# Kernel optimization log

Hardware: AMD Instinct MI355X
Metric: run time of the kernel (lower is better)

## Reference

```python
import jax, jax.numpy as jnp
import numpy as np

K = 512
H = 8

def setup_inputs() -> dict:
    key = jax.random.key(0)
    k1, k2, k3, k4, k5 = jax.random.split(key, 5)
    b, s = 2, 2048
    x = jax.random.normal(k1, (b, s, K), dtype=jnp.float32)
    # torch Linear weights: shape [out_features, in_features]
    scale = 0.02
    Wq = jax.random.normal(k2, (H * K, K), dtype=jnp.float32) * scale
    Wk = jax.random.normal(k3, (H * K, K), dtype=jnp.float32) * scale
    Wv = jax.random.normal(k4, (H * K, K), dtype=jnp.float32) * scale
    Wu = jax.random.normal(k5, (K, H * K), dtype=jnp.float32) * scale
    return {"x": x, "Wq": Wq, "Wk": Wk, "Wv": Wv, "Wu": Wu}

def reference(x, Wq, Wk, Wv, Wu):
    b, s, _ = x.shape
    # project and split heads: [b, h, s, k]
    q = jnp.einsum('bsd,hed->bhse', x, Wq.reshape(H, K, K))
    kk = jnp.einsum('bsd,hed->bhse', x, Wk.reshape(H, K, K))
    v = jnp.einsum('bsd,hed->bhse', x, Wv.reshape(H, K, K))
    scale = K ** (-0.25)
    dot = jnp.einsum('bhse,bhte->bhst', q * scale, kk * scale)  # [b,h,s,s]
    causal = jnp.tril(jnp.ones((s, s), dtype=bool))
    dot = jnp.where(causal[None, None], dot, -jnp.inf)
    weights = jax.nn.softmax(dot, axis=-1)
    heads_out = jnp.einsum('bhst,bhte->bhse', weights, v)  # [b,h,s,k]
    heads_out = heads_out.transpose(0, 2, 1, 3).reshape(b, s, H * K)
    return heads_out @ Wu.T
```

## Files before the change

### kernel.cpp

```cpp
#include <hip/hip_runtime.h>
#include <hip/hip_bf16.h>
#include <cstdint>
#include <cstddef>


typedef __bf16 bf16;
typedef __bf16 bf16x8 __attribute__((ext_vector_type(8)));
typedef float  f32x4  __attribute__((ext_vector_type(4)));
typedef unsigned short u16x4 __attribute__((ext_vector_type(4)));

__device__ __forceinline__ void gl2lds16(const void* g, void* l) {
  __builtin_amdgcn_global_load_lds(
      (const __attribute__((address_space(1))) unsigned int*)g,
      (__attribute__((address_space(3))) unsigned int*)l, 16, 0, 0);
}

__device__ __forceinline__ unsigned short bfbits(float f) {
  return __builtin_bit_cast(unsigned short, (__bf16)f);
}

__global__ __launch_bounds__(256) void cvt_all(
    const float* __restrict__ x,  const float* __restrict__ wq,
    const float* __restrict__ wk, const float* __restrict__ wv,
    const float* __restrict__ wu,
    bf16* __restrict__ xb,  bf16* __restrict__ wqb, bf16* __restrict__ wkb,
    bf16* __restrict__ wvb, bf16* __restrict__ wub)
{
  const int Q4 = (1 << 21) / 4;
  int i = blockIdx.x * 256 + threadIdx.x;
  int a = i / Q4;
  int off = (i - a * Q4) * 4;
  const float* s; bf16* d;
  switch (a) {
    case 0: s = x;  d = xb;  break;
    case 1: s = wq; d = wqb; break;
    case 2: s = wk; d = wkb; break;
    case 3: s = wv; d = wvb; break;
    default: s = wu; d = wub; break;
  }
  float4 v = *(const float4*)(s + off);
  u16x4 o = { bfbits(v.x), bfbits(v.y), bfbits(v.z), bfbits(v.w) };
  *(u16x4*)(d + off) = o;
}

template<int BM, int BN, int MODE>
__global__ __launch_bounds__((BM >= 256 ? 2 : BM / 64) * (BN / 64) * 64)
void gemm_bt(const bf16* __restrict__ A, const bf16* __restrict__ B,
             void* __restrict__ Cp, int M, int N, int K)
{
  constexpr int BK = 32;
  constexpr int WM = (BM >= 256 ? 128 : 64);
  constexpr int MI = WM / 16;
  constexpr int WAVES_M = BM / WM;
  constexpr int WAVES_N = BN / 64;
  constexpr int NT = WAVES_M * WAVES_N * 64;
  __shared__ __align__(16) bf16 lds[2][(BM + BN) * BK];

  const int tid = threadIdx.x, w = tid >> 6, lane = tid & 63;
  const int g = lane >> 4, c16 = lane & 15;
  const int q8 = gridDim.x >> 3;
  const int wg = (blockIdx.x & 7) * q8 + (blockIdx.x >> 3);
  const int nbn = N / BN;
  const int bm = wg / nbn, bn = wg % nbn;
  const int m0 = bm * BM, n0 = bn * BN;
  const int wr = w / WAVES_N, wc = w % WAVES_N;

  f32x4 z = {0.f, 0.f, 0.f, 0.f};
  f32x4 acc[MI][4];
  #pragma unroll
  for (int i = 0; i < MI; i++)
    #pragma unroll
    for (int j = 0; j < 4; j++) acc[i][j] = z;

  const int nk = K / BK;

  auto stage = [&](int buf, int kt) {
    bf16* la = &lds[buf][0];
    #pragma unroll
    for (int r = 0; r < (BM * BK / 8) / NT; r++) {
      int c = r * NT + tid;
      int row = c >> 2, p = c & 3, s = p ^ ((row >> 1) & 3);
      gl2lds16(A + (size_t)(m0 + row) * K + (size_t)kt * BK + s * 8,
               la + (r * NT + w * 64) * 8);
    }
    bf16* lb = &lds[buf][BM * BK];
    #pragma unroll
    for (int r = 0; r < (BN * BK / 8) / NT; r++) {
      int c = r * NT + tid;
      int row = c >> 2, p = c & 3, s = p ^ ((row >> 1) & 3);
      gl2lds16(B + (size_t)(n0 + row) * K + (size_t)kt * BK + s * 8,
               lb + (r * NT + w * 64) * 8);
    }
  };

  stage(0, 0);
  __syncthreads();
  int cur = 0;
  for (int kt = 0; kt < nk; ++kt) {
    if (kt + 1 < nk) stage(cur ^ 1, kt + 1);
    const bf16* lA = &lds[cur][0];
    const bf16* lB = &lds[cur][BM * BK];
    bf16x8 af[MI], bfv[4];
    #pragma unroll
    for (int i = 0; i < MI; i++) {
      int ra = wr * WM + i * 16 + c16;
      af[i] = *(const bf16x8*)&lA[ra * BK + ((g ^ ((ra >> 1) & 3)) * 8)];
    }
    #pragma unroll
    for (int j = 0; j < 4; j++) {
      int rb = wc * 64 + j * 16 + c16;
      bfv[j] = *(const bf16x8*)&lB[rb * BK + ((g ^ ((rb >> 1) & 3)) * 8)];
    }
    #pragma unroll
    for (int i = 0; i < MI; i++)
      #pragma unroll
      for (int j = 0; j < 4; j++)
        acc[i][j] = __builtin_amdgcn_mfma_f32_16x16x32_bf16(af[i], bfv[j],
                                                            acc[i][j], 0, 0, 0);
    __syncthreads();
    cur ^= 1;
  }

  if constexpr (MODE == 0) {
    bf16* C = (bf16*)Cp;
    #pragma unroll
    for (int i = 0; i < MI; i++) {
      int mg = m0 + wr * WM + i * 16 + g * 4;
      #pragma unroll
      for (int j = 0; j < 4; j++) {
        int ng = n0 + wc * 64 + j * 16 + c16;
        #pragma unroll
        for (int jj = 0; jj < 4; jj++)
          C[(size_t)(mg + jj) * N + ng] = (bf16)acc[i][j][jj];
      }
    }
  } else if constexpr (MODE == 1) {
    bf16* C = (bf16*)Cp;
    #pragma unroll
    for (int i = 0; i < MI; i++) {
      int mg = m0 + wr * WM + i * 16 + g * 4;
      int bb = mg >> 11, srow = mg & 2047;
      #pragma unroll
      for (int j = 0; j < 4; j++) {
        int ng = n0 + wc * 64 + j * 16 + c16;
        u16x4 pk = { bfbits(acc[i][j][0]), bfbits(acc[i][j][1]),
                     bfbits(acc[i][j][2]), bfbits(acc[i][j][3]) };
        *(u16x4*)&C[(size_t)(bb * 4096 + ng) * 2048 + srow] = pk;
      }
    }
  } else {
    float* C = (float*)Cp;
    #pragma unroll
    for (int i = 0; i < MI; i++) {
      int mg = m0 + wr * WM + i * 16 + g * 4;
      #pragma unroll
      for (int j = 0; j < 4; j++) {
        int ng = n0 + wc * 64 + j * 16 + c16;
        #pragma unroll
        for (int jj = 0; jj < 4; jj++)
          C[(size_t)(mg + jj) * N + ng] = acc[i][j][jj];
      }
    }
  }
}

__global__ __launch_bounds__(512)
void sgemm_causal(const bf16* __restrict__ Qb, const bf16* __restrict__ Kb,
                  bf16* __restrict__ Sp, float* __restrict__ l)
{
  constexpr int BK = 32;
  __shared__ __align__(16) bf16 lds[2][512 * BK];
  const int tid = threadIdx.x, w = tid >> 6, lane = tid & 63;
  const int g = lane >> 4, c16 = lane & 15;

  const int wg = (blockIdx.x & 7) * 72 + (blockIdx.x >> 3);
  const int bh = wg / 36, t = wg % 36;
  int TM = 0;
  while ((TM + 1) * (TM + 2) / 2 <= t) TM++;
  const int TN = t - TM * (TM + 1) / 2;
  const int b = bh >> 3, h = bh & 7;
  const bf16* Ab = Qb + (size_t)(b * 2048 + TM * 256) * 4096 + h * 512;
  const bf16* Bb = Kb + (size_t)(b * 2048 + TN * 256) * 4096 + h * 512;
  const int wr = w >> 2, wc = w & 3;

  f32x4 z = {0.f, 0.f, 0.f, 0.f};
  f32x4 acc[8][4];
  #pragma unroll
  for (int i = 0; i < 8; i++)
    #pragma unroll
    for (int j = 0; j < 4; j++) acc[i][j] = z;

  auto stage = [&](int buf, int kt) {
    bf16* la = &lds[buf][0];
    #pragma unroll
    for (int r = 0; r < 2; r++) {
      int c = r * 512 + tid;
      int row = c >> 2, p = c & 3, s = p ^ ((row >> 1) & 3);
      gl2lds16(Ab + (size_t)row * 4096 + kt * BK + s * 8,
               la + (r * 512 + w * 64) * 8);
    }
    bf16* lb = &lds[buf][256 * BK];
    #pragma unroll
    for (int r = 0; r < 2; r++) {
      int c = r * 512 + tid;
      int row = c >> 2, p = c & 3, s = p ^ ((row >> 1) & 3);
      gl2lds16(Bb + (size_t)row * 4096 + kt * BK + s * 8,
               lb + (r * 512 + w * 64) * 8);
    }
  };

  stage(0, 0);
  __syncthreads();
  int cur = 0;
  for (int kt = 0; kt < 16; ++kt) {
    if (kt + 1 < 16) stage(cur ^ 1, kt + 1);
    const bf16* lA = &lds[cur][0];
    const bf16* lB = &lds[cur][256 * BK];
    bf16x8 af[8], bfv[4];
    #pragma unroll
    for (int i = 0; i < 8; i++) {
      int ra = wr * 128 + i * 16 + c16;
      af[i] = *(const bf16x8*)&lA[ra * BK + ((g ^ ((ra >> 1) & 3)) * 8)];
    }
    #pragma unroll
    for (int j = 0; j < 4; j++) {
      int rb = wc * 64 + j * 16 + c16;
      bfv[j] = *(const bf16x8*)&lB[rb * BK + ((g ^ ((rb >> 1) & 3)) * 8)];
    }
    #pragma unroll
    for (int i = 0; i < 8; i++)
      #pragma unroll
      for (int j = 0; j < 4; j++)
        acc[i][j] = __builtin_amdgcn_mfma_f32_16x16x32_bf16(af[i], bfv[j],
                                                            acc[i][j], 0, 0, 0);
    __syncthreads();
    cur ^= 1;
  }

  const float SC2 = 0.044194173824159216f * 1.4426950408889634f;
  bf16* spb = Sp + (size_t)bh * 136 * 16384;
  float rsum[8][4];
  #pragma unroll
  for (int i = 0; i < 8; i++)
    #pragma unroll
    for (int jj = 0; jj < 4; jj++) rsum[i][jj] = 0.f;

  #pragma unroll
  for (int i = 0; i < 8; i++) {
    #pragma unroll
    for (int j = 0; j < 4; j++) {
      int kl = wc * 64 + j * 16 + c16;
      int kglob = TN * 256 + kl;
      int tn128 = kglob >> 7, kc = kglob & 127;
      #pragma unroll
      for (int jj = 0; jj < 4; jj++) {
        int ml = wr * 128 + i * 16 + g * 4 + jj;
        int qglob = TM * 256 + ml;
        float p = (kglob <= qglob) ? exp2f(acc[i][j][jj] * SC2) : 0.f;
        rsum[i][jj] += p;
        int tm128 = qglob >> 7;
        if (tn128 <= tm128)
          spb[(size_t)(tm128 * (tm128 + 1) / 2 + tn128) * 16384
              + (qglob & 127) * 128 + kc] = (bf16)p;
      }
    }
  }
  #pragma unroll
  for (int i = 0; i < 8; i++)
    #pragma unroll
    for (int jj = 0; jj < 4; jj++) {
      float v = rsum[i][jj];
      v += __shfl_xor(v, 1);
      v += __shfl_xor(v, 2);
      v += __shfl_xor(v, 4);
      v += __shfl_xor(v, 8);
      if (c16 == 0) {
        int qglob = TM * 256 + wr * 128 + i * 16 + g * 4 + jj;
        atomicAdd(&l[bh * 2048 + qglob], v);
      }
    }
}

__global__ __launch_bounds__(512)
void pv_gemm(const bf16* __restrict__ Pp, const bf16* __restrict__ Vt,
             const float* __restrict__ l, bf16* __restrict__ HO)
{
  constexpr int BK = 32;
  __shared__ __align__(16) bf16 lds[2][384 * BK];
  __shared__ float sInv[128];
  const int tid = threadIdx.x, w = tid >> 6, lane = tid & 63;
  const int g = lane >> 4, c16 = lane & 15;

  const int wg = (blockIdx.x & 7) * 64 + (blockIdx.x >> 3);
  const int bh = wg >> 5, r5 = wg & 31;
  const int tm = 15 - (r5 >> 1), nd = r5 & 1;
  const int b = bh >> 3, h = bh & 7;
  const size_t pb = (size_t)bh * 136 + (size_t)tm * (tm + 1) / 2;
  const bf16* Bb = Vt + (size_t)(bh * 512 + nd * 256) * 2048;
  const int wr = w >> 2, wc = w & 3;
  const int nk = (tm + 1) * 4;

  f32x4 z = {0.f, 0.f, 0.f, 0.f};
  f32x4 acc[4][4];
  #pragma unroll
  for (int i = 0; i < 4; i++)
    #pragma unroll
    for (int j = 0; j < 4; j++) acc[i][j] = z;

  auto stage = [&](int buf, int kt) {
    const bf16* At = Pp + (pb + (kt >> 2)) * 16384 + (kt & 3) * 32;
    bf16* la = &lds[buf][0];
    {
      int row = tid >> 2, p = tid & 3, s = p ^ ((row >> 1) & 3);
      gl2lds16(At + (size_t)row * 128 + s * 8, la + (w * 64) * 8);
    }
    bf16* lb = &lds[buf][128 * BK];
    #pragma unroll
    for (int r = 0; r < 2; r++) {
      int c = r * 512 + tid;
      int row = c >> 2, p = c & 3, s = p ^ ((row >> 1) & 3);
      gl2lds16(Bb + (size_t)row * 2048 + kt * BK + s * 8,
               lb + (r * 512 + w * 64) * 8);
    }
  };

  stage(0, 0);
  if (tid < 128) sInv[tid] = 1.0f / l[bh * 2048 + tm * 128 + tid];
  __syncthreads();
  int cur = 0;
  for (int kt = 0; kt < nk; ++kt) {
    if (kt + 1 < nk) stage(cur ^ 1, kt + 1);
    const bf16* lA = &lds[cur][0];
    const bf16* lB = &lds[cur][128 * BK];
    bf16x8 af[4], bfv[4];
    #pragma unroll
    for (int i = 0; i < 4; i++) {
      int ra = wr * 64 + i * 16 + c16;
      af[i] = *(const bf16x8*)&lA[ra * BK + ((g ^ ((ra >> 1) & 3)) * 8)];
    }
    #pragma unroll
    for (int j = 0; j < 4; j++) {
      int rb = wc * 64 + j * 16 + c16;
      bfv[j] = *(const bf16x8*)&lB[rb * BK + ((g ^ ((rb >> 1) & 3)) * 8)];
    }
    #pragma unroll
    for (int i = 0; i < 4; i++)
      #pragma unroll
      for (int j = 0; j < 4; j++)
        acc[i][j] = __builtin_amdgcn_mfma_f32_16x16x32_bf16(af[i], bfv[j],
                                                            acc[i][j], 0, 0, 0);
    __syncthreads();
    cur ^= 1;
  }

  bf16* Cb = HO + (size_t)(b * 2048 + tm * 128) * 4096 + h * 512 + nd * 256;
  #pragma unroll
  for (int i = 0; i < 4; i++) {
    int ml = wr * 64 + i * 16 + g * 4;
    #pragma unroll
    for (int j = 0; j < 4; j++) {
      int nl = wc * 64 + j * 16 + c16;
      #pragma unroll
      for (int jj = 0; jj < 4; jj++)
        Cb[(size_t)(ml + jj) * 4096 + nl] =
            (bf16)(acc[i][j][jj] * sInv[ml + jj]);
    }
  }
}

extern "C" void kernel_launch(void* const* d_in, const int* in_sizes, int n_in,
                              void* d_out, int out_size, void* d_ws,
                              size_t ws_size, hipStream_t stream)
{
  (void)in_sizes; (void)n_in; (void)out_size; (void)ws_size;
  const float* x  = (const float*)d_in[0];
  const float* wq = (const float*)d_in[1];
  const float* wk = (const float*)d_in[2];
  const float* wv = (const float*)d_in[3];
  const float* wu = (const float*)d_in[4];

  char* ws = (char*)d_ws;
  const size_t MB = 1024 * 1024;
  bf16*  wub = (bf16*)(ws + 0 * MB);
  float* lR  = (float*)(ws + 4 * MB);
  bf16*  Qb  = (bf16*)(ws + 5 * MB);
  bf16*  Kbf = (bf16*)(ws + 37 * MB);
  bf16*  Sp  = (bf16*)(ws + 69 * MB);
  bf16*  wqb = (bf16*)(ws + 69 * MB);
  bf16*  wkb = (bf16*)(ws + 73 * MB);
  bf16*  xb  = (bf16*)(ws + 137 * MB);
  bf16*  wvb = (bf16*)(ws + 141 * MB);
  bf16*  Vtb = Kbf;
  bf16*  HOb = Qb;

  hipMemsetAsync(lR, 0, 16 * 2048 * sizeof(float), stream);
  hipLaunchKernelGGL(cvt_all, dim3(10240), dim3(256), 0, stream,
                     x, wq, wk, wv, wu, xb, wqb, wkb, wvb, wub);
  hipLaunchKernelGGL((gemm_bt<256, 256, 0>), dim3(256), dim3(512), 0, stream,
                     xb, wqb, (void*)Qb, 4096, 4096, 512);
  hipLaunchKernelGGL((gemm_bt<256, 256, 0>), dim3(256), dim3(512), 0, stream,
                     xb, wkb, (void*)Kbf, 4096, 4096, 512);
  hipLaunchKernelGGL(sgemm_causal, dim3(576), dim3(512), 0, stream,
                     Qb, Kbf, Sp, lR);
  hipLaunchKernelGGL((gemm_bt<256, 256, 1>), dim3(256), dim3(512), 0, stream,
                     xb, wvb, (void*)Vtb, 4096, 4096, 512);
  hipLaunchKernelGGL(pv_gemm, dim3(512), dim3(512), 0, stream,
                     Sp, Vtb, lR, HOb);
  hipLaunchKernelGGL((gemm_bt<128, 64, 2>), dim3(256), dim3(128), 0, stream,
                     HOb, wub, d_out, 4096, 512, 4096);
}
```

Before: 371.7 us.

## Stage GEMM epilogues through LDS for coalesced vector global stores

The projection GEMM, QK^T/softmax and PV kernels now write accumulator tiles into padded shared memory, in half-tiles, and then copy them out with 16-byte row-contiguous global stores. Before, each lane wrote scattered 2- or 4-byte elements, which made poorly coalesced store traffic for the large Q/K/V, P and head-output buffers. The shared buffer is sized to the larger of the staging and epilogue needs, and the extra barriers add synchronisation cost. The final output projection GEMM also changes its tile shape from 128x64 to 64x128, which now covers 128 columns per block.

```diff
diff --git a/kernel.cpp b/kernel.cpp
--- a/kernel.cpp
+++ b/kernel.cpp
@@ -54,7 +54,12 @@
   constexpr int WAVES_M = BM / WM;
   constexpr int WAVES_N = BN / 64;
   constexpr int NT = WAVES_M * WAVES_N * 64;
-  __shared__ __align__(16) bf16 lds[2][(BM + BN) * BK];
+  constexpr int STG = 2 * (BM + BN) * BK;
+  constexpr int EPE = (MODE == 0) ? 128 * 264
+                    : (MODE == 1) ? 256 * 136
+                    : 64 * 132 * 2;
+  constexpr int SME = STG > EPE ? STG : EPE;
+  __shared__ __align__(16) bf16 smem[SME];
 
   const int tid = threadIdx.x, w = tid >> 6, lane = tid & 63;
   const int g = lane >> 4, c16 = lane & 15;
@@ -75,7 +80,7 @@
   const int nk = K / BK;
 
   auto stage = [&](int buf, int kt) {
-    bf16* la = &lds[buf][0];
+    bf16* la = &smem[buf * (BM + BN) * BK];
     #pragma unroll
     for (int r = 0; r < (BM * BK / 8) / NT; r++) {
       int c = r * NT + tid;
@@ -83,7 +88,7 @@
       gl2lds16(A + (size_t)(m0 + row) * K + (size_t)kt * BK + s * 8,
                la + (r * NT + w * 64) * 8);
     }
-    bf16* lb = &lds[buf][BM * BK];
+    bf16* lb = &smem[buf * (BM + BN) * BK + BM * BK];
     #pragma unroll
     for (int r = 0; r < (BN * BK / 8) / NT; r++) {
       int c = r * NT + tid;
@@ -98,8 +103,8 @@
   int cur = 0;
   for (int kt = 0; kt < nk; ++kt) {
     if (kt + 1 < nk) stage(cur ^ 1, kt + 1);
-    const bf16* lA = &lds[cur][0];
-    const bf16* lB = &lds[cur][BM * BK];
+    const bf16* lA = &smem[cur * (BM + BN) * BK];
+    const bf16* lB = &smem[cur * (BM + BN) * BK + BM * BK];
     bf16x8 af[MI], bfv[4];
     #pragma unroll
     for (int i = 0; i < MI; i++) {
@@ -122,44 +127,87 @@
   }
 
   if constexpr (MODE == 0) {
+    bf16* ep = smem;
+    #pragma unroll
+    for (int hp = 0; hp < 2; ++hp) {
+      if (wr == hp) {
+        #pragma unroll
+        for (int i = 0; i < MI; i++) {
+          int rl = i * 16 + g * 4;
+          #pragma unroll
+          for (int j = 0; j < 4; j++) {
+            int cl = wc * 64 + j * 16 + c16;
+            #pragma unroll
+            for (int jj = 0; jj < 4; jj++)
+              ep[(rl + jj) * 264 + cl] = (bf16)acc[i][j][jj];
+          }
+        }
+      }
+      __syncthreads();
+      {
+        bf16* C = (bf16*)Cp;
+        int r = tid >> 2, ch = tid & 3;
+        const bf16* src = &ep[r * 264 + ch * 64];
+        bf16* dst = C + (size_t)(m0 + hp * 128 + r) * N + n0 + ch * 64;
+        #pragma unroll
+        for (int q = 0; q < 8; q++)
+          *(bf16x8*)(dst + q * 8) = *(const bf16x8*)(src + q * 8);
+      }
+      if (hp == 0) __syncthreads();
+    }
+  } else if constexpr (MODE == 1) {
+    bf16* ep = smem;
     bf16* C = (bf16*)Cp;
     #pragma unroll
+    for (int hp = 0; hp < 2; ++hp) {
+      if (wr == hp) {
+        #pragma unroll
+        for (int i = 0; i < MI; i++) {
+          int rl = i * 16 + g * 4;
+          #pragma unroll
+          for (int j = 0; j < 4; j++) {
+            int cl = wc * 64 + j * 16 + c16;
+            u16x4 pk = { bfbits(acc[i][j][0]), bfbits(acc[i][j][1]),
+                         bfbits(acc[i][j][2]), bfbits(acc[i][j][3]) };
+            *(u16x4*)&ep[cl * 136 + rl] = pk;
+          }
+        }
+      }
+      __syncthreads();
+      {
+        int cl = tid >> 1, rc = tid & 1;
+        const bf16* src = &ep[cl * 136 + rc * 64];
+        int mg = m0 + hp * 128 + rc * 64;
+        int bb = mg >> 11, srow = mg & 2047;
+        bf16* dst = C + ((size_t)(bb * 4096 + n0 + cl)) * 2048 + srow;
+        #pragma unroll
+        for (int q = 0; q < 8; q++)
+          *(bf16x8*)(dst + q * 8) = *(const bf16x8*)(src + q * 8);
+      }
+      if (hp == 0) __syncthreads();
+    }
+  } else {
+    float* ep = (float*)smem;
+    #pragma unroll
     for (int i = 0; i < MI; i++) {
-      int mg = m0 + wr * WM + i * 16 + g * 4;
+      int rl = i * 16 + g * 4;
       #pragma unroll
       for (int j = 0; j < 4; j++) {
-        int ng = n0 + wc * 64 + j * 16 + c16;
+        int cl = wc * 64 + j * 16 + c16;
         #pragma unroll
         for (int jj = 0; jj < 4; jj++)
-          C[(size_t)(mg + jj) * N + ng] = (bf16)acc[i][j][jj];
-      }
-    }
-  } else if constexpr (MODE == 1) {
-    bf16* C = (bf16*)Cp;
-    #pragma unroll
-    for (int i = 0; i < MI; i++) {
-      int mg = m0 + wr * WM + i * 16 + g * 4;
-      int bb = mg >> 11, srow = mg & 2047;
-      #pragma unroll
-      for (int j = 0; j < 4; j++) {
-        int ng = n0 + wc * 64 + j * 16 + c16;
-        u16x4 pk = { bfbits(acc[i][j][0]), bfbits(acc[i][j][1]),
-                     bfbits(acc[i][j][2]), bfbits(acc[i][j][3]) };
-        *(u16x4*)&C[(size_t)(bb * 4096 + ng) * 2048 + srow] = pk;
-      }
-    }
-  } else {
-    float* C = (float*)Cp;
-    #pragma unroll
-    for (int i = 0; i < MI; i++) {
-      int mg = m0 + wr * WM + i * 16 + g * 4;
-      #pragma unroll
-      for (int j = 0; j < 4; j++) {
-        int ng = n0 + wc * 64 + j * 16 + c16;
-        #pragma unroll
-        for (int jj = 0; jj < 4; jj++)
-          C[(size_t)(mg + jj) * N + ng] = acc[i][j][jj];
-      }
+          ep[(rl + jj) * 132 + cl] = acc[i][j][jj];
+      }
+    }
+    __syncthreads();
+    {
+      float* C = (float*)Cp;
+      int r = tid >> 1, ch = tid & 1;
+      const float* src = &ep[r * 132 + ch * 64];
+      float* dst = C + (size_t)(m0 + r) * N + n0 + ch * 64;
+      #pragma unroll
+      for (int q = 0; q < 16; q++)
+        *(float4*)(dst + q * 4) = *(const float4*)(src + q * 4);
     }
   }
 }
@@ -169,7 +217,9 @@
                   bf16* __restrict__ Sp, float* __restrict__ l)
 {
   constexpr int BK = 32;
-  __shared__ __align__(16) bf16 lds[2][512 * BK];
+  constexpr int STG = 2 * 512 * BK;
+  constexpr int EPE = 128 * 264;
+  __shared__ __align__(16) bf16 smem[EPE > STG ? EPE : STG];
   const int tid = threadIdx.x, w = tid >> 6, lane = tid & 63;
   const int g = lane >> 4, c16 = lane & 15;
 
@@ -191,7 +241,7 @@
     for (int j = 0; j < 4; j++) acc[i][j] = z;
 
   auto stage = [&](int buf, int kt) {
-    bf16* la = &lds[buf][0];
+    bf16* la = &smem[buf * 16384];
     #pragma unroll
     for (int r = 0; r < 2; r++) {
       int c = r * 512 + tid;
@@ -199,7 +249,7 @@
       gl2lds16(Ab + (size_t)row * 4096 + kt * BK + s * 8,
                la + (r * 512 + w * 64) * 8);
     }
-    bf16* lb = &lds[buf][256 * BK];
+    bf16* lb = &smem[buf * 16384 + 256 * BK];
     #pragma unroll
     for (int r = 0; r < 2; r++) {
       int c = r * 512 + tid;
@@ -214,8 +264,8 @@
   int cur = 0;
   for (int kt = 0; kt < 16; ++kt) {
     if (kt + 1 < 16) stage(cur ^ 1, kt + 1);
-    const bf16* lA = &lds[cur][0];
-    const bf16* lB = &lds[cur][256 * BK];
+    const bf16* lA = &smem[cur * 16384];
+    const bf16* lB = &smem[cur * 16384 + 256 * BK];
     bf16x8 af[8], bfv[4];
     #pragma unroll
     for (int i = 0; i < 8; i++) {
@@ -239,6 +289,7 @@
 
   const float SC2 = 0.044194173824159216f * 1.4426950408889634f;
   bf16* spb = Sp + (size_t)bh * 136 * 16384;
+  bf16* ep = smem;
   float rsum[8][4];
   #pragma unroll
   for (int i = 0; i < 8; i++)
@@ -246,25 +297,41 @@
     for (int jj = 0; jj < 4; jj++) rsum[i][jj] = 0.f;
 
   #pragma unroll
-  for (int i = 0; i < 8; i++) {
-    #pragma unroll
-    for (int j = 0; j < 4; j++) {
-      int kl = wc * 64 + j * 16 + c16;
-      int kglob = TN * 256 + kl;
-      int tn128 = kglob >> 7, kc = kglob & 127;
-      #pragma unroll
-      for (int jj = 0; jj < 4; jj++) {
-        int ml = wr * 128 + i * 16 + g * 4 + jj;
-        int qglob = TM * 256 + ml;
-        float p = (kglob <= qglob) ? exp2f(acc[i][j][jj] * SC2) : 0.f;
-        rsum[i][jj] += p;
-        int tm128 = qglob >> 7;
-        if (tn128 <= tm128)
-          spb[(size_t)(tm128 * (tm128 + 1) / 2 + tn128) * 16384
-              + (qglob & 127) * 128 + kc] = (bf16)p;
-      }
-    }
-  }
+  for (int hp = 0; hp < 2; ++hp) {
+    if (wr == hp) {
+      #pragma unroll
+      for (int i = 0; i < 8; i++) {
+        #pragma unroll
+        for (int j = 0; j < 4; j++) {
+          int cl = wc * 64 + j * 16 + c16;
+          int kglob = TN * 256 + cl;
+          #pragma unroll
+          for (int jj = 0; jj < 4; jj++) {
+            int rl = i * 16 + g * 4 + jj;
+            int qglob = TM * 256 + hp * 128 + rl;
+            float p = (kglob <= qglob) ? exp2f(acc[i][j][jj] * SC2) : 0.f;
+            rsum[i][jj] += p;
+            ep[rl * 264 + cl] = (bf16)p;
+          }
+        }
+      }
+    }
+    __syncthreads();
+    {
+      int r = tid >> 2, ch = tid & 3;
+      int tm128 = 2 * TM + hp, tn128 = 2 * TN + (ch >> 1);
+      if (tn128 <= tm128) {
+        const bf16* src = &ep[r * 264 + ch * 64];
+        bf16* dst = spb + (size_t)(tm128 * (tm128 + 1) / 2 + tn128) * 16384
+                    + r * 128 + (ch & 1) * 64;
+        #pragma unroll
+        for (int q = 0; q < 8; q++)
+          *(bf16x8*)(dst + q * 8) = *(const bf16x8*)(src + q * 8);
+      }
+    }
+    if (hp == 0) __syncthreads();
+  }
+
   #pragma unroll
   for (int i = 0; i < 8; i++)
     #pragma unroll
@@ -286,7 +353,8 @@
              const float* __restrict__ l, bf16* __restrict__ HO)
 {
   constexpr int BK = 32;
-  __shared__ __align__(16) bf16 lds[2][384 * BK];
+  constexpr int STG = 2 * 384 * BK;
+  __shared__ __align__(16) bf16 smem[STG];
   __shared__ float sInv[128];
   const int tid = threadIdx.x, w = tid >> 6, lane = tid & 63;
   const int g = lane >> 4, c16 = lane & 15;
@@ -294,7 +362,7 @@
   const int wg = (blockIdx.x & 7) * 64 + (blockIdx.x >> 3);
   const int bh = wg >> 5, r5 = wg & 31;
   const int tm = 15 - (r5 >> 1), nd = r5 & 1;
-  const int b = bh >> 3, h = bh & 7;
+  const int b = bh >> 3, hh = bh & 7;
   const size_t pb = (size_t)bh * 136 + (size_t)tm * (tm + 1) / 2;
   const bf16* Bb = Vt + (size_t)(bh * 512 + nd * 256) * 2048;
   const int wr = w >> 2, wc = w & 3;
@@ -309,12 +377,12 @@
 
   auto stage = [&](int buf, int kt) {
     const bf16* At = Pp + (pb + (kt >> 2)) * 16384 + (kt & 3) * 32;
-    bf16* la = &lds[buf][0];
+    bf16* la = &smem[buf * 12288];
     {
       int row = tid >> 2, p = tid & 3, s = p ^ ((row >> 1) & 3);
       gl2lds16(At + (size_t)row * 128 + s * 8, la + (w * 64) * 8);
     }
-    bf16* lb = &lds[buf][128 * BK];
+    bf16* lb = &smem[buf * 12288 + 128 * BK];
     #pragma unroll
     for (int r = 0; r < 2; r++) {
       int c = r * 512 + tid;
@@ -330,8 +398,8 @@
   int cur = 0;
   for (int kt = 0; kt < nk; ++kt) {
     if (kt + 1 < nk) stage(cur ^ 1, kt + 1);
-    const bf16* lA = &lds[cur][0];
-    const bf16* lB = &lds[cur][128 * BK];
+    const bf16* lA = &smem[cur * 12288];
+    const bf16* lB = &smem[cur * 12288 + 128 * BK];
     bf16x8 af[4], bfv[4];
     #pragma unroll
     for (int i = 0; i < 4; i++) {
@@ -353,18 +421,35 @@
     cur ^= 1;
   }
 
-  bf16* Cb = HO + (size_t)(b * 2048 + tm * 128) * 4096 + h * 512 + nd * 256;
-  #pragma unroll
-  for (int i = 0; i < 4; i++) {
-    int ml = wr * 64 + i * 16 + g * 4;
-    #pragma unroll
-    for (int j = 0; j < 4; j++) {
-      int nl = wc * 64 + j * 16 + c16;
-      #pragma unroll
-      for (int jj = 0; jj < 4; jj++)
-        Cb[(size_t)(ml + jj) * 4096 + nl] =
-            (bf16)(acc[i][j][jj] * sInv[ml + jj]);
-    }
+  bf16* Cb = HO + (size_t)(b * 2048 + tm * 128) * 4096 + hh * 512 + nd * 256;
+  bf16* ep = smem;
+  #pragma unroll
+  for (int hp = 0; hp < 2; ++hp) {
+    if (wr == hp) {
+      #pragma unroll
+      for (int i = 0; i < 4; i++) {
+        #pragma unroll
+        for (int j = 0; j < 4; j++) {
+          int cl = wc * 64 + j * 16 + c16;
+          #pragma unroll
+          for (int jj = 0; jj < 4; jj++) {
+            int rl = i * 16 + g * 4 + jj;
+            ep[rl * 264 + cl] =
+                (bf16)(acc[i][j][jj] * sInv[hp * 64 + rl]);
+          }
+        }
+      }
+    }
+    __syncthreads();
+    {
+      int r = tid >> 3, ch = tid & 7;
+      const bf16* src = &ep[r * 264 + ch * 32];
+      bf16* dst = Cb + (size_t)(hp * 64 + r) * 4096 + ch * 32;
+      #pragma unroll
+      for (int q = 0; q < 4; q++)
+        *(bf16x8*)(dst + q * 8) = *(const bf16x8*)(src + q * 8);
+    }
+    if (hp == 0) __syncthreads();
   }
 }
 
@@ -406,6 +491,6 @@
                      xb, wvb, (void*)Vtb, 4096, 4096, 512);
   hipLaunchKernelGGL(pv_gemm, dim3(512), dim3(512), 0, stream,
                      Sp, Vtb, lR, HOb);
-  hipLaunchKernelGGL((gemm_bt<128, 64, 2>), dim3(256), dim3(128), 0, stream,
+  hipLaunchKernelGGL((gemm_bt<64, 128, 2>), dim3(256), dim3(128), 0, stream,
                      HOb, wub, d_out, 4096, 512, 4096);
 }
```

Result: slower. 402.8 us (+8.4%).
